# Optimization experiments

Measured on AMD Instinct MI355X. Metric: run time of the kernel, lower is better.

Reference implementation:

```python
import jax, jax.numpy as jnp
import numpy as np

N = 50000      # nodes
K = 12         # neighbors per node (regular graph, required by e.view(-1, numNgbrs))
E = N * K      # edges, sorted by row
F_IN = 128
F_OUT = 128
ALPHA = 0.2    # LeakyReLU negative slope


def setup_inputs() -> dict:
    key = jax.random.key(0)
    k_x, k_col, k_ws, k_wn, k_a, k_b = jax.random.split(key, 6)
    x = jax.random.normal(k_x, (N, F_IN), dtype=jnp.float32)
    # edges sorted by destination row, exactly K per node
    row = jnp.repeat(jnp.arange(N, dtype=jnp.int32), K)
    col = jax.random.randint(k_col, (E,), 0, N, dtype=jnp.int32)
    adj_vals = jnp.ones((E,), dtype=jnp.float32)  # sparse adj values
    stdv = 1.0 / np.sqrt(F_OUT)
    W_self = jax.random.uniform(k_ws, (F_IN, F_OUT), jnp.float32, -stdv, stdv)
    W_neighbor = jax.random.uniform(k_wn, (F_IN, F_OUT), jnp.float32, -stdv, stdv)
    lim = 1.414 * np.sqrt(6.0 / (2 * F_OUT + 1))  # xavier_uniform gain=1.414 on [2F,1]
    a = jax.random.uniform(k_a, (2 * F_OUT,), jnp.float32, -lim, lim)
    bias = jax.random.uniform(k_b, (F_OUT,), jnp.float32, -stdv, stdv)
    return {"x": x, "adj_vals": adj_vals, "row": row, "col": col,
            "W_self": W_self, "W_neighbor": W_neighbor, "a": a, "bias": bias}


def reference(x, adj_vals, row, col, W_self, W_neighbor, a, bias):
    act_self = x @ W_self                       # [N, F_OUT]
    h = x @ W_neighbor                          # [N, F_OUT]
    # cat([h_in, h_out], 1) @ a  ==  h_in @ a[:F] + h_out @ a[F:]
    # precompute per-node dots, then gather per edge (cheaper than ExF gathers)
    s_in = h @ a[:F_OUT]                        # [N]
    s_out = h @ a[F_OUT:]                       # [N]
    e = jax.nn.leaky_relu(s_in[row] + s_out[col], ALPHA)   # [E]
    # per-destination-node softmax over its K contiguous edges
    att = jax.nn.softmax(e.reshape(N, K), axis=1).reshape(-1)  # [E]
    # attention-weighted sparse scatter-add aggregation
    msg = (adj_vals * att)[:, None] * h[col]    # [E, F_OUT]
    act_neighbor = jax.ops.segment_sum(msg, row, num_segments=N)
    return act_self + act_neighbor + bias
```

## Files before the change

kernel.cpp:

```cpp
#include <hip/hip_runtime.h>

constexpr int N_NODES = 50000;
constexpr int KNB = 12;
constexpr int F = 128;
constexpr float ALPHA = 0.2f;
constexpr int BM = 64;

typedef __bf16 bf16x8 __attribute__((ext_vector_type(8)));
typedef float  f32x4  __attribute__((ext_vector_type(4)));

__device__ __forceinline__ unsigned bfr(float f) {
    unsigned u = __float_as_uint(f);
    return (u + 0x7fffu + ((u >> 16) & 1u)) >> 16;
}
__device__ __forceinline__ unsigned pack2(float lo, float hi) {
    return bfr(lo) | (bfr(hi) << 16);
}
__device__ __forceinline__ float bf2f(unsigned bits16) {
    return __uint_as_float(bits16 << 16);
}

__global__ __launch_bounds__(256) void gat_prep(const float* __restrict__ Wself,
                                                const float* __restrict__ Wnb,
                                                unsigned* __restrict__ Wt) {
    const int gid = blockIdx.x * 256 + threadIdx.x;
    const int n  = gid >> 6;
    const int kp = gid & 63;
    const int k16 = kp >> 2;
    const int sub = kp & 3;
    const float* src = (n < F) ? (Wself + n) : (Wnb + (n - F));
    const float f0 = src[(size_t)(kp * 2)     * F];
    const float f1 = src[(size_t)(kp * 2 + 1) * F];
    Wt[n * 64 + (k16 ^ (n & 7)) * 4 + sub] = pack2(f0, f1);
}

__global__ __launch_bounds__(256, 2) void gat_gemm(
    const float* __restrict__ x,
    const unsigned* __restrict__ Wt,
    const float* __restrict__ a,
    const float* __restrict__ bias,
    float* __restrict__ out,
    unsigned short* __restrict__ hb,
    float* __restrict__ s_in,
    float* __restrict__ s_out)
{
    __shared__ uint4 ldsX[BM * 16];
    __shared__ uint4 ldsW[256 * 16];

    const int t = threadIdx.x;
    const int w    = t >> 6;
    const int lane = t & 63;
    const int base = blockIdx.x * BM;

    const uint4* Wt4 = reinterpret_cast<const uint4*>(Wt);
#pragma unroll
    for (int i = 0; i < 16; ++i) {
        const int ch = w * 16 + i;
        const uint4* gp = Wt4 + ch * 64 + lane;
        uint4* lp = ldsW + ch * 64;
        __builtin_amdgcn_global_load_lds(
            (const __attribute__((address_space(1))) void*)gp,
            (__attribute__((address_space(3))) void*)lp, 16, 0, 0);
    }
#pragma unroll
    for (int i = 0; i < 4; ++i) {
        const int idx = t + i * 256;
        const int row = idx >> 4;
        const int k16 = idx & 15;
        int gr = base + row; if (gr >= N_NODES) gr = N_NODES - 1;
        const float4* xp = reinterpret_cast<const float4*>(x + (size_t)gr * F + k16 * 8);
        const float4 f0 = xp[0];
        const float4 f1 = xp[1];
        uint4 v;
        v.x = pack2(f0.x, f0.y); v.y = pack2(f0.z, f0.w);
        v.z = pack2(f1.x, f1.y); v.w = pack2(f1.z, f1.w);
        ldsX[row * 16 + (k16 ^ (row & 7))] = v;
    }
    __syncthreads();

    const int lq   = lane >> 4;
    const int lr   = lane & 15;

    const bf16x8* fx = reinterpret_cast<const bf16x8*>(ldsX);
    const bf16x8* fw = reinterpret_cast<const bf16x8*>(ldsW);

    f32x4 acc[4][4];
#pragma unroll
    for (int mt = 0; mt < 4; ++mt)
#pragma unroll
        for (int rt = 0; rt < 4; ++rt)
            acc[mt][rt] = f32x4{0.f, 0.f, 0.f, 0.f};

#pragma unroll
    for (int s = 0; s < 4; ++s) {
        bf16x8 wf[4], xf[4];
#pragma unroll
        for (int mt = 0; mt < 4; ++mt) {
            const int n = w * 64 + mt * 16 + lr;
            wf[mt] = fw[n * 16 + ((s * 4 + lq) ^ (n & 7))];
        }
#pragma unroll
        for (int rt = 0; rt < 4; ++rt) {
            const int r = rt * 16 + lr;
            xf[rt] = fx[r * 16 + ((s * 4 + lq) ^ (r & 7))];
        }
#pragma unroll
        for (int mt = 0; mt < 4; ++mt)
#pragma unroll
            for (int rt = 0; rt < 4; ++rt)
                acc[mt][rt] = __builtin_amdgcn_mfma_f32_16x16x32_bf16(wf[mt], xf[rt], acc[mt][rt], 0, 0, 0);
    }

    __syncthreads();
    float* sbuf = reinterpret_cast<float*>(ldsX);

    if (w < 2) {
#pragma unroll
        for (int mt = 0; mt < 4; ++mt) {
            const int col0 = w * 64 + mt * 16 + lq * 4;
            const float4 b4 = *reinterpret_cast<const float4*>(bias + col0);
#pragma unroll
            for (int rt = 0; rt < 4; ++rt) {
                const int row = base + rt * 16 + lr;
                if (row < N_NODES) {
                    const f32x4 v = acc[mt][rt];
                    float4 o{v[0] + b4.x, v[1] + b4.y, v[2] + b4.z, v[3] + b4.w};
                    *reinterpret_cast<float4*>(out + (size_t)row * F + col0) = o;
                }
            }
        }
    } else {
        float spin[4] = {0.f, 0.f, 0.f, 0.f};
        float spout[4] = {0.f, 0.f, 0.f, 0.f};
#pragma unroll
        for (int mt = 0; mt < 4; ++mt) {
            const int colh0 = (w - 2) * 64 + mt * 16 + lq * 4;
            const float4 al = *reinterpret_cast<const float4*>(a + colh0);
            const float4 ah = *reinterpret_cast<const float4*>(a + F + colh0);
#pragma unroll
            for (int rt = 0; rt < 4; ++rt) {
                const int row = base + rt * 16 + lr;
                const f32x4 v = acc[mt][rt];
                if (row < N_NODES) {
                    uint2 pk{pack2(v[0], v[1]), pack2(v[2], v[3])};
                    *reinterpret_cast<uint2*>(hb + (size_t)row * F + colh0) = pk;
                }
                spin[rt]  = fmaf(v[0], al.x, fmaf(v[1], al.y, fmaf(v[2], al.z, fmaf(v[3], al.w, spin[rt]))));
                spout[rt] = fmaf(v[0], ah.x, fmaf(v[1], ah.y, fmaf(v[2], ah.z, fmaf(v[3], ah.w, spout[rt]))));
            }
        }
#pragma unroll
        for (int rt = 0; rt < 4; ++rt) {
            spin[rt]  += __shfl_xor(spin[rt], 16);
            spin[rt]  += __shfl_xor(spin[rt], 32);
            spout[rt] += __shfl_xor(spout[rt], 16);
            spout[rt] += __shfl_xor(spout[rt], 32);
        }
        if (lq == 0) {
#pragma unroll
            for (int rt = 0; rt < 4; ++rt) {
                sbuf[(w - 2) * 128 + rt * 16 + lr]      = spin[rt];
                sbuf[(w - 2) * 128 + 64 + rt * 16 + lr] = spout[rt];
            }
        }
    }
    __syncthreads();
    if (t < 128) {
        const int i = t & 63;
        const int row = base + i;
        if (row < N_NODES) {
            if (t < 64) s_in[row]  = sbuf[i] + sbuf[128 + i];
            else        s_out[row] = sbuf[64 + i] + sbuf[192 + i];
        }
    }
}

__global__ __launch_bounds__(256) void gat_attn(
    const uint4* __restrict__ hbU4,
    const float* __restrict__ s_in,
    const float* __restrict__ s_out,
    const int* __restrict__ colidx,
    const float* __restrict__ adj,
    float* __restrict__ out)
{
    const int wid  = threadIdx.x >> 6;
    const int lane = threadIdx.x & 63;
    const int lr   = lane & 15;
    const int node = (blockIdx.x * 4 + wid) * 4 + (lane >> 4);

    float e = -1e30f;
    int c = 0;
    float av = 0.f;
    if (lr < KNB) {
        c  = colidx[node * KNB + lr];
        av = adj[node * KNB + lr];
        const float ev = s_in[node] + s_out[c];
        e = ev > 0.f ? ev : ALPHA * ev;
    }
    float m = e;
#pragma unroll
    for (int msk = 8; msk >= 1; msk >>= 1) m = fmaxf(m, __shfl_xor(m, msk));
    const float p = (lr < KNB) ? __expf(e - m) : 0.f;
    float ssum = p;
#pragma unroll
    for (int msk = 8; msk >= 1; msk >>= 1) ssum += __shfl_xor(ssum, msk);
    const float att = p / ssum * av;

    float accf[8];
#pragma unroll
    for (int k = 0; k < 8; ++k) accf[k] = 0.f;
    const int gbase = lane & 48;
#pragma unroll
    for (int j = 0; j < KNB; ++j) {
        const float aj = __shfl(att, gbase + j);
        const int   cj = __shfl(c,   gbase + j);
        const uint4 u = hbU4[(size_t)cj * 16 + lr];
        accf[0] = fmaf(aj, bf2f(u.x & 0xffffu), accf[0]);
        accf[1] = fmaf(aj, bf2f(u.x >> 16),     accf[1]);
        accf[2] = fmaf(aj, bf2f(u.y & 0xffffu), accf[2]);
        accf[3] = fmaf(aj, bf2f(u.y >> 16),     accf[3]);
        accf[4] = fmaf(aj, bf2f(u.z & 0xffffu), accf[4]);
        accf[5] = fmaf(aj, bf2f(u.z >> 16),     accf[5]);
        accf[6] = fmaf(aj, bf2f(u.w & 0xffffu), accf[6]);
        accf[7] = fmaf(aj, bf2f(u.w >> 16),     accf[7]);
    }
    float4* op = reinterpret_cast<float4*>(out + (size_t)node * F + lr * 8);
    float4 o0 = op[0];
    float4 o1 = op[1];
    o0.x += accf[0]; o0.y += accf[1]; o0.z += accf[2]; o0.w += accf[3];
    o1.x += accf[4]; o1.y += accf[5]; o1.z += accf[6]; o1.w += accf[7];
    op[0] = o0;
    op[1] = o1;
}

extern "C" void kernel_launch(void* const* d_in, const int* in_sizes, int n_in,
                              void* d_out, int out_size, void* d_ws, size_t ws_size,
                              hipStream_t stream) {
    const float* x     = (const float*)d_in[0];
    const float* adj   = (const float*)d_in[1];
    const int*   col   = (const int*)d_in[3];
    const float* Wself = (const float*)d_in[4];
    const float* Wnb   = (const float*)d_in[5];
    const float* a     = (const float*)d_in[6];
    const float* bias  = (const float*)d_in[7];
    float* out = (float*)d_out;

    char* ws = (char*)d_ws;
    unsigned short* hb = (unsigned short*)ws;
    float* s_in  = (float*)(ws + 12800000);
    float* s_out = (float*)(ws + 13000000);
    unsigned* Wt = (unsigned*)(ws + 13200000);

    gat_prep<<<64, 256, 0, stream>>>(Wself, Wnb, Wt);
    gat_gemm<<<(N_NODES + BM - 1) / BM, 256, 0, stream>>>(x, Wt, a, bias, out, hb, s_in, s_out);
    gat_attn<<<(N_NODES + 15) / 16, 256, 0, stream>>>((const uint4*)hb, s_in, s_out, col, adj, out);
}
```

Baseline: 57.14 us.

## Store self-term as bf16 intermediate and loop two tiles per GEMM block

The GEMM kernel now writes the self projection plus bias as bf16 to a workspace buffer instead of fp32 to the output. The attention kernel then reads that buffer and writes the output once, with no read-modify-write. This cuts the self-term traffic in half and removes one full fp32 read of the output. Each GEMM block also handles two 64-row tiles, which amortises the weight load into LDS but halves the block count and adds extra barriers. The self term loses precision because it is rounded to bf16.

```diff
diff --git a/kernel.cpp b/kernel.cpp
--- a/kernel.cpp
+++ b/kernel.cpp
@@ -5,6 +5,7 @@
 constexpr int F = 128;
 constexpr float ALPHA = 0.2f;
 constexpr int BM = 64;
+constexpr int TILES_PER_BLK = 2;
 
 typedef __bf16 bf16x8 __attribute__((ext_vector_type(8)));
 typedef float  f32x4  __attribute__((ext_vector_type(4)));
@@ -39,7 +40,7 @@
     const unsigned* __restrict__ Wt,
     const float* __restrict__ a,
     const float* __restrict__ bias,
-    float* __restrict__ out,
+    unsigned short* __restrict__ selfb,
     unsigned short* __restrict__ hb,
     float* __restrict__ s_in,
     float* __restrict__ s_out)
@@ -50,7 +51,8 @@
     const int t = threadIdx.x;
     const int w    = t >> 6;
     const int lane = t & 63;
-    const int base = blockIdx.x * BM;
+    const int lq   = lane >> 4;
+    const int lr   = lane & 15;
 
     const uint4* Wt4 = reinterpret_cast<const uint4*>(Wt);
 #pragma unroll
@@ -62,121 +64,125 @@
             (const __attribute__((address_space(1))) void*)gp,
             (__attribute__((address_space(3))) void*)lp, 16, 0, 0);
     }
-#pragma unroll
-    for (int i = 0; i < 4; ++i) {
-        const int idx = t + i * 256;
-        const int row = idx >> 4;
-        const int k16 = idx & 15;
-        int gr = base + row; if (gr >= N_NODES) gr = N_NODES - 1;
-        const float4* xp = reinterpret_cast<const float4*>(x + (size_t)gr * F + k16 * 8);
-        const float4 f0 = xp[0];
-        const float4 f1 = xp[1];
-        uint4 v;
-        v.x = pack2(f0.x, f0.y); v.y = pack2(f0.z, f0.w);
-        v.z = pack2(f1.x, f1.y); v.w = pack2(f1.z, f1.w);
-        ldsX[row * 16 + (k16 ^ (row & 7))] = v;
-    }
-    __syncthreads();
-
-    const int lq   = lane >> 4;
-    const int lr   = lane & 15;
 
     const bf16x8* fx = reinterpret_cast<const bf16x8*>(ldsX);
     const bf16x8* fw = reinterpret_cast<const bf16x8*>(ldsW);
-
-    f32x4 acc[4][4];
-#pragma unroll
-    for (int mt = 0; mt < 4; ++mt)
-#pragma unroll
-        for (int rt = 0; rt < 4; ++rt)
-            acc[mt][rt] = f32x4{0.f, 0.f, 0.f, 0.f};
-
-#pragma unroll
-    for (int s = 0; s < 4; ++s) {
-        bf16x8 wf[4], xf[4];
-#pragma unroll
-        for (int mt = 0; mt < 4; ++mt) {
-            const int n = w * 64 + mt * 16 + lr;
-            wf[mt] = fw[n * 16 + ((s * 4 + lq) ^ (n & 7))];
-        }
-#pragma unroll
-        for (int rt = 0; rt < 4; ++rt) {
-            const int r = rt * 16 + lr;
-            xf[rt] = fx[r * 16 + ((s * 4 + lq) ^ (r & 7))];
-        }
+    float* sbuf = reinterpret_cast<float*>(ldsX);
+
+    for (int it = 0; it < TILES_PER_BLK; ++it) {
+        const int base = (blockIdx.x * TILES_PER_BLK + it) * BM;
+
+#pragma unroll
+        for (int i = 0; i < 4; ++i) {
+            const int idx = t + i * 256;
+            const int row = idx >> 4;
+            const int k16 = idx & 15;
+            int gr = base + row; if (gr >= N_NODES) gr = N_NODES - 1;
+            const float4* xp = reinterpret_cast<const float4*>(x + (size_t)gr * F + k16 * 8);
+            const float4 f0 = xp[0];
+            const float4 f1 = xp[1];
+            uint4 v;
+            v.x = pack2(f0.x, f0.y); v.y = pack2(f0.z, f0.w);
+            v.z = pack2(f1.x, f1.y); v.w = pack2(f1.z, f1.w);
+            ldsX[row * 16 + (k16 ^ (row & 7))] = v;
+        }
+        __syncthreads();
+
+        f32x4 acc[4][4];
 #pragma unroll
         for (int mt = 0; mt < 4; ++mt)
 #pragma unroll
             for (int rt = 0; rt < 4; ++rt)
-                acc[mt][rt] = __builtin_amdgcn_mfma_f32_16x16x32_bf16(wf[mt], xf[rt], acc[mt][rt], 0, 0, 0);
-    }
-
-    __syncthreads();
-    float* sbuf = reinterpret_cast<float*>(ldsX);
-
-    if (w < 2) {
-#pragma unroll
-        for (int mt = 0; mt < 4; ++mt) {
-            const int col0 = w * 64 + mt * 16 + lq * 4;
-            const float4 b4 = *reinterpret_cast<const float4*>(bias + col0);
+                acc[mt][rt] = f32x4{0.f, 0.f, 0.f, 0.f};
+
+#pragma unroll
+        for (int s = 0; s < 4; ++s) {
+            bf16x8 wf[4], xf[4];
+#pragma unroll
+            for (int mt = 0; mt < 4; ++mt) {
+                const int n = w * 64 + mt * 16 + lr;
+                wf[mt] = fw[n * 16 + ((s * 4 + lq) ^ (n & 7))];
+            }
 #pragma unroll
             for (int rt = 0; rt < 4; ++rt) {
-                const int row = base + rt * 16 + lr;
-                if (row < N_NODES) {
+                const int r = rt * 16 + lr;
+                xf[rt] = fx[r * 16 + ((s * 4 + lq) ^ (r & 7))];
+            }
+#pragma unroll
+            for (int mt = 0; mt < 4; ++mt)
+#pragma unroll
+                for (int rt = 0; rt < 4; ++rt)
+                    acc[mt][rt] = __builtin_amdgcn_mfma_f32_16x16x32_bf16(wf[mt], xf[rt], acc[mt][rt], 0, 0, 0);
+        }
+
+        __syncthreads();
+
+        if (w < 2) {
+#pragma unroll
+            for (int mt = 0; mt < 4; ++mt) {
+                const int col0 = w * 64 + mt * 16 + lq * 4;
+                const float4 b4 = *reinterpret_cast<const float4*>(bias + col0);
+#pragma unroll
+                for (int rt = 0; rt < 4; ++rt) {
+                    const int row = base + rt * 16 + lr;
+                    if (row < N_NODES) {
+                        const f32x4 v = acc[mt][rt];
+                        uint2 pk{pack2(v[0] + b4.x, v[1] + b4.y), pack2(v[2] + b4.z, v[3] + b4.w)};
+                        *reinterpret_cast<uint2*>(selfb + (size_t)row * F + col0) = pk;
+                    }
+                }
+            }
+        } else {
+            float spin[4] = {0.f, 0.f, 0.f, 0.f};
+            float spout[4] = {0.f, 0.f, 0.f, 0.f};
+#pragma unroll
+            for (int mt = 0; mt < 4; ++mt) {
+                const int colh0 = (w - 2) * 64 + mt * 16 + lq * 4;
+                const float4 al = *reinterpret_cast<const float4*>(a + colh0);
+                const float4 ah = *reinterpret_cast<const float4*>(a + F + colh0);
+#pragma unroll
+                for (int rt = 0; rt < 4; ++rt) {
+                    const int row = base + rt * 16 + lr;
                     const f32x4 v = acc[mt][rt];
-                    float4 o{v[0] + b4.x, v[1] + b4.y, v[2] + b4.z, v[3] + b4.w};
-                    *reinterpret_cast<float4*>(out + (size_t)row * F + col0) = o;
+                    if (row < N_NODES) {
+                        uint2 pk{pack2(v[0], v[1]), pack2(v[2], v[3])};
+                        *reinterpret_cast<uint2*>(hb + (size_t)row * F + colh0) = pk;
+                    }
+                    spin[rt]  = fmaf(v[0], al.x, fmaf(v[1], al.y, fmaf(v[2], al.z, fmaf(v[3], al.w, spin[rt]))));
+                    spout[rt] = fmaf(v[0], ah.x, fmaf(v[1], ah.y, fmaf(v[2], ah.z, fmaf(v[3], ah.w, spout[rt]))));
                 }
             }
-        }
-    } else {
-        float spin[4] = {0.f, 0.f, 0.f, 0.f};
-        float spout[4] = {0.f, 0.f, 0.f, 0.f};
-#pragma unroll
-        for (int mt = 0; mt < 4; ++mt) {
-            const int colh0 = (w - 2) * 64 + mt * 16 + lq * 4;
-            const float4 al = *reinterpret_cast<const float4*>(a + colh0);
-            const float4 ah = *reinterpret_cast<const float4*>(a + F + colh0);
 #pragma unroll
             for (int rt = 0; rt < 4; ++rt) {
-                const int row = base + rt * 16 + lr;
-                const f32x4 v = acc[mt][rt];
-                if (row < N_NODES) {
-                    uint2 pk{pack2(v[0], v[1]), pack2(v[2], v[3])};
-                    *reinterpret_cast<uint2*>(hb + (size_t)row * F + colh0) = pk;
+                spin[rt]  += __shfl_xor(spin[rt], 16);
+                spin[rt]  += __shfl_xor(spin[rt], 32);
+                spout[rt] += __shfl_xor(spout[rt], 16);
+                spout[rt] += __shfl_xor(spout[rt], 32);
+            }
+            if (lq == 0) {
+#pragma unroll
+                for (int rt = 0; rt < 4; ++rt) {
+                    sbuf[(w - 2) * 128 + rt * 16 + lr]      = spin[rt];
+                    sbuf[(w - 2) * 128 + 64 + rt * 16 + lr] = spout[rt];
                 }
-                spin[rt]  = fmaf(v[0], al.x, fmaf(v[1], al.y, fmaf(v[2], al.z, fmaf(v[3], al.w, spin[rt]))));
-                spout[rt] = fmaf(v[0], ah.x, fmaf(v[1], ah.y, fmaf(v[2], ah.z, fmaf(v[3], ah.w, spout[rt]))));
-            }
-        }
-#pragma unroll
-        for (int rt = 0; rt < 4; ++rt) {
-            spin[rt]  += __shfl_xor(spin[rt], 16);
-            spin[rt]  += __shfl_xor(spin[rt], 32);
-            spout[rt] += __shfl_xor(spout[rt], 16);
-            spout[rt] += __shfl_xor(spout[rt], 32);
-        }
-        if (lq == 0) {
-#pragma unroll
-            for (int rt = 0; rt < 4; ++rt) {
-                sbuf[(w - 2) * 128 + rt * 16 + lr]      = spin[rt];
-                sbuf[(w - 2) * 128 + 64 + rt * 16 + lr] = spout[rt];
-            }
-        }
-    }
-    __syncthreads();
-    if (t < 128) {
-        const int i = t & 63;
-        const int row = base + i;
-        if (row < N_NODES) {
-            if (t < 64) s_in[row]  = sbuf[i] + sbuf[128 + i];
-            else        s_out[row] = sbuf[64 + i] + sbuf[192 + i];
-        }
+            }
+        }
+        __syncthreads();
+        if (t < 128) {
+            const int i = t & 63;
+            const int row = base + i;
+            if (row < N_NODES) {
+                if (t < 64) s_in[row]  = sbuf[i] + sbuf[128 + i];
+                else        s_out[row] = sbuf[64 + i] + sbuf[192 + i];
+            }
+        }
+        __syncthreads();
     }
 }
 
 __global__ __launch_bounds__(256) void gat_attn(
     const uint4* __restrict__ hbU4,
+    const uint4* __restrict__ selfbU4,
     const float* __restrict__ s_in,
     const float* __restrict__ s_out,
     const int* __restrict__ colidx,
@@ -206,9 +212,13 @@
     for (int msk = 8; msk >= 1; msk >>= 1) ssum += __shfl_xor(ssum, msk);
     const float att = p / ssum * av;
 
+    const uint4 sb = selfbU4[(size_t)node * 16 + lr];
     float accf[8];
-#pragma unroll
-    for (int k = 0; k < 8; ++k) accf[k] = 0.f;
+    accf[0] = bf2f(sb.x & 0xffffu); accf[1] = bf2f(sb.x >> 16);
+    accf[2] = bf2f(sb.y & 0xffffu); accf[3] = bf2f(sb.y >> 16);
+    accf[4] = bf2f(sb.z & 0xffffu); accf[5] = bf2f(sb.z >> 16);
+    accf[6] = bf2f(sb.w & 0xffffu); accf[7] = bf2f(sb.w >> 16);
+
     const int gbase = lane & 48;
 #pragma unroll
     for (int j = 0; j < KNB; ++j) {
@@ -225,12 +235,8 @@
         accf[7] = fmaf(aj, bf2f(u.w >> 16),     accf[7]);
     }
     float4* op = reinterpret_cast<float4*>(out + (size_t)node * F + lr * 8);
-    float4 o0 = op[0];
-    float4 o1 = op[1];
-    o0.x += accf[0]; o0.y += accf[1]; o0.z += accf[2]; o0.w += accf[3];
-    o1.x += accf[4]; o1.y += accf[5]; o1.z += accf[6]; o1.w += accf[7];
-    op[0] = o0;
-    op[1] = o1;
+    op[0] = float4{accf[0], accf[1], accf[2], accf[3]};
+    op[1] = float4{accf[4], accf[5], accf[6], accf[7]};
 }
 
 extern "C" void kernel_launch(void* const* d_in, const int* in_sizes, int n_in,
@@ -246,12 +252,16 @@
     float* out = (float*)d_out;
 
     char* ws = (char*)d_ws;
-    unsigned short* hb = (unsigned short*)ws;
-    float* s_in  = (float*)(ws + 12800000);
-    float* s_out = (float*)(ws + 13000000);
-    unsigned* Wt = (unsigned*)(ws + 13200000);
+    unsigned short* hb    = (unsigned short*)ws;
+    unsigned short* selfb = (unsigned short*)(ws + 12800000);
+    float* s_in  = (float*)(ws + 25600000);
+    float* s_out = (float*)(ws + 25800000);
+    unsigned* Wt = (unsigned*)(ws + 26000000);
 
     gat_prep<<<64, 256, 0, stream>>>(Wself, Wnb, Wt);
-    gat_gemm<<<(N_NODES + BM - 1) / BM, 256, 0, stream>>>(x, Wt, a, bias, out, hb, s_in, s_out);
-    gat_attn<<<(N_NODES + 15) / 16, 256, 0, stream>>>((const uint4*)hb, s_in, s_out, col, adj, out);
-}
+    const int ntiles = (N_NODES + BM - 1) / BM;
+    const int nblk   = (ntiles + TILES_PER_BLK - 1) / TILES_PER_BLK;
+    gat_gemm<<<nblk, 256, 0, stream>>>(x, Wt, a, bias, selfb, hb, s_in, s_out);
+    gat_attn<<<(N_NODES + 15) / 16, 256, 0, stream>>>((const uint4*)hb, (const uint4*)selfb,
+                                                      s_in, s_out, col, adj, out);
+}
```

Result: faster. 52.98 us (-7.3%).
